# Kernel tuning notes

Hardware: AMD Instinct MI355X
Metric: run time of the kernel (lower is better)

Reference implementation:

```python
import jax, jax.numpy as jnp
import numpy as np
from jax import lax

NUM_EXPERT = 2   # top-k experts kept per image
N_EXPERTS = 4    # total experts


def setup_inputs() -> dict:
    key = jax.random.key(0)
    ks = jax.random.split(key, 4)
    B, C, H, W = 16, 64, 128, 128
    inputs = jax.random.normal(ks[0], (B, C, H, W), dtype=jnp.float32)
    k = jax.random.uniform(ks[1], (B, C, 1, 1), dtype=jnp.float32)
    gate_w = jax.random.normal(ks[2], (N_EXPERTS, C), dtype=jnp.float32) * (1.0 / np.sqrt(C))
    gate_b = jnp.zeros((N_EXPERTS,), dtype=jnp.float32)
    conv_w = jax.random.normal(ks[3], (N_EXPERTS, C, C, 3, 3), dtype=jnp.float32) * (1.0 / np.sqrt(C * 9))
    conv_b = jnp.zeros((N_EXPERTS, C), dtype=jnp.float32)
    return {"inputs": inputs, "k": k, "gate_w": gate_w, "gate_b": gate_b,
            "conv_w": conv_w, "conv_b": conv_b}


def _expert(x, k, w, b):
    # expert_i(x, k) = ReLU(Conv3x3_i(x) + b_i) * k   (FiLM-style conditioning)
    y = lax.conv_general_dilated(x, w, window_strides=(1, 1), padding='SAME',
                                 dimension_numbers=('NCHW', 'OIHW', 'NCHW'))
    return jax.nn.relu(y + b[None, :, None, None]) * k


def reference(inputs, k, gate_w, gate_b, conv_w, conv_b):
    B = inputs.shape[0]
    # gate: global average pool over HW, then linear C -> E
    pooled = inputs.mean(axis=(2, 3))                       # [B, C]
    logits = pooled @ gate_w.T + gate_b                     # [B, E]
    # softmax in float32 (matches F.softmax(..., dtype=torch.float))
    weights = jax.nn.softmax(logits.astype(jnp.float32), axis=1).astype(inputs.dtype)
    topk_w, topk_idx = lax.top_k(weights, NUM_EXPERT)       # [B, num_expert]
    # scatter top-k weights into a dense [B, E] mask (zeros elsewhere)
    exp_weights = jnp.zeros_like(weights).at[jnp.arange(B)[:, None], topk_idx].set(topk_w)
    # dense loop over ALL experts, weighted sum with mostly-zero weights
    out = inputs
    for i in range(N_EXPERTS):
        out = out + _expert(inputs, k, conv_w[i], conv_b[i]) * exp_weights[:, i, None, None, None]
    return out
```

## Files before the change

### kernel.cpp

```cpp
#include <hip/hip_runtime.h>

typedef __attribute__((ext_vector_type(8))) short bfrag8;
typedef __attribute__((ext_vector_type(4))) short bfrag4;
typedef __attribute__((ext_vector_type(16))) float f32x16;

#define B_ 16
#define C_ 64
#define H_ 128
#define W_ 128
#define E_ 4
#define HW_ (H_ * W_)

#define NSL 66
#define PLANE2 (NSL * 16)
#define ROWB2  (8 * PLANE2)
#define RGK 16

#define WT_ELEMS (4 * 9 * 2 * 4 * 64 * 8)
#define OFF_POOL (WT_ELEMS * 2)
#define OFF_EW   (OFF_POOL + 1024 * 4)
#define WS_NEEDED ((size_t)(OFF_EW + 64 * 4))

#define FB_WT_OFF 0
#define FB_POOLED_OFF 147456
#define FB_EW_OFF 148480

__device__ inline unsigned short f2bf(float f) {
    unsigned u = __builtin_bit_cast(unsigned, f);
    unsigned r = u + 0x7FFFu + ((u >> 16) & 1u);
    return (unsigned short)(r >> 16);
}
__device__ inline float bf2f(unsigned short s) {
    return __builtin_bit_cast(float, (unsigned)s << 16);
}

__global__ __launch_bounds__(256) void pool_wcvt(const float* __restrict__ in,
                                                 const float* __restrict__ cw,
                                                 float* __restrict__ pooled,
                                                 unsigned short* __restrict__ wT2) {
    if (blockIdx.x < 576) {
        const int idx = blockIdx.x * 256 + threadIdx.x;
        const int j = idx & 7;
        const int l = (idx >> 3) & 63;
        const int f = idx >> 9;
        const int kb = f & 3;
        const int chh = (f >> 2) & 1;
        const int et = f >> 3;
        const int tap = et % 9;
        const int e = et / 9;
        const int co = chh * 32 + (l & 31);
        const int ci = kb * 16 + (l >> 5) * 8 + j;
        wT2[idx] = f2bf(cw[(((e * C_ + co) * C_ + ci) * 9) + tap]);
    }
    const int bc = blockIdx.x;
    const float* p = in + (size_t)bc * HW_;
    float s = 0.f;
    for (int i = threadIdx.x; i < HW_ / 4; i += 256) {
        float4 v = ((const float4*)p)[i];
        s += v.x + v.y + v.z + v.w;
    }
    for (int off = 32; off; off >>= 1) s += __shfl_down(s, off);
    __shared__ float red[4];
    const int lane = threadIdx.x & 63, wv = threadIdx.x >> 6;
    if (lane == 0) red[wv] = s;
    __syncthreads();
    if (threadIdx.x == 0)
        pooled[bc] = (red[0] + red[1] + red[2] + red[3]) * (1.0f / (float)HW_);
}

__global__ void gate_kernel(const float* __restrict__ pooled,
                            const float* __restrict__ gate_w,
                            const float* __restrict__ gate_b,
                            float* __restrict__ ew) {
    const int b = threadIdx.x;
    if (b >= B_) return;
    float lg[E_];
    for (int e = 0; e < E_; e++) {
        float s = gate_b[e];
        for (int c = 0; c < C_; c++) s += pooled[b * C_ + c] * gate_w[e * C_ + c];
        lg[e] = s;
    }
    float m = fmaxf(fmaxf(lg[0], lg[1]), fmaxf(lg[2], lg[3]));
    float ex[E_], sum = 0.f;
    for (int e = 0; e < E_; e++) { ex[e] = expf(lg[e] - m); sum += ex[e]; }
    for (int e = 0; e < E_; e++) ex[e] /= sum;
    int i1 = 0;
    for (int e = 1; e < E_; e++) if (ex[e] > ex[i1]) i1 = e;
    int i2 = -1;
    for (int e = 0; e < E_; e++) {
        if (e == i1) continue;
        if (i2 < 0 || ex[e] > ex[i2]) i2 = e;
    }
    for (int e = 0; e < E_; e++)
        ew[b * E_ + e] = (e == i1 || e == i2) ? ex[e] : 0.f;
}

__global__ __launch_bounds__(512, 1) void conv_pin(const float* __restrict__ in,
                                                   const float* __restrict__ kk,
                                                   const float* __restrict__ cb,
                                                   const float* __restrict__ pooled,
                                                   const float* __restrict__ gw,
                                                   const float* __restrict__ gb,
                                                   const unsigned short* __restrict__ wT2,
                                                   float* __restrict__ out) {
    const int raw = blockIdx.x;
    const int swz = (raw & 7) * 32 + (raw >> 3);
    const int b   = swz >> 4;
    const int pxh = (swz >> 3) & 1;
    const int h0  = (swz & 7) * RGK;
    const int x0g = pxh * 64;

    const int tid = threadIdx.x;
    const int lane = tid & 63;
    const int wv = tid >> 6;
    const int ln = lane & 31;
    const int lh = lane >> 5;
    const int ei = wv >> 2;
    const int ch = (wv >> 1) & 1;
    const int pq = wv & 1;
    const int co0 = ch * 32;

    const int spx = tid & 63;
    const int scg = tid >> 6;

    __shared__ __align__(16) char ring[3 * ROWB2];
    __shared__ float pbuf[2 * 2 * 32 * 32];
    __shared__ float sEW[E_];

    if (tid < 64) {
        const float p = pooled[b * C_ + lane];
        float part[E_];
#pragma unroll
        for (int e = 0; e < E_; e++) part[e] = p * gw[e * C_ + lane];
#pragma unroll
        for (int off = 32; off; off >>= 1)
#pragma unroll
            for (int e = 0; e < E_; e++) part[e] += __shfl_down(part[e], off);
        if (lane == 0) {
            float lg[E_];
#pragma unroll
            for (int e = 0; e < E_; e++) lg[e] = part[e] + gb[e];
            float m = fmaxf(fmaxf(lg[0], lg[1]), fmaxf(lg[2], lg[3]));
            float ex[E_], sum = 0.f;
#pragma unroll
            for (int e = 0; e < E_; e++) { ex[e] = __expf(lg[e] - m); sum += ex[e]; }
            const float inv = 1.0f / sum;
            int i1 = 0;
            for (int e = 1; e < E_; e++) if (ex[e] > ex[i1]) i1 = e;
            int i2 = -1;
            for (int e = 0; e < E_; e++) {
                if (e == i1) continue;
                if (i2 < 0 || ex[e] > ex[i2]) i2 = e;
            }
#pragma unroll
            for (int e = 0; e < E_; e++)
                sEW[e] = (e == i1 || e == i2) ? ex[e] * inv : 0.f;
        }
    }
    __syncthreads();

    int e0 = 0, e1 = 0; float w0 = 0.f, w1 = 0.f;
    {
        int found = 0;
        for (int e = 0; e < E_; e++) {
            float we = sEW[e];
            if (we != 0.f) {
                if (!found) { e0 = e; w0 = we; found = 1; }
                else        { e1 = e; w1 = we; }
            }
        }
        if (w1 == 0.f) e1 = e0;
    }

    const int es = ei ? e1 : e0;
    const float ww = ei ? w1 : w0;
    const float* cbp = cb + es * C_;
    const float* kkp = kk + b * C_;

    bfrag8 wr[9][4];
    {
        const char* wb = (const char*)wT2 + (size_t)es * 73728 + ch * 4096 + lane * 16;
#pragma unroll
        for (int tap = 0; tap < 9; ++tap)
#pragma unroll
            for (int kb = 0; kb < 4; ++kb)
                wr[tap][kb] = *(const bfrag8*)(wb + tap * 8192 + kb * 1024);
    }
#pragma unroll
    for (int tap = 0; tap < 9; ++tap)
#pragma unroll
        for (int kb = 0; kb < 4; ++kb)
            asm volatile("" : "+v"(wr[tap][kb]));

    float pv[8], ph[8];
    auto STAGE = [&](int r) {
        if ((unsigned)r < (unsigned)H_) {
            const float* src = in + ((size_t)(b * C_ + scg * 8) * H_ + r) * W_ + x0g + spx;
#pragma unroll
            for (int i = 0; i < 8; ++i) pv[i] = src[(size_t)i * HW_];
        } else {
#pragma unroll
            for (int i = 0; i < 8; ++i) pv[i] = 0.f;
        }
        if (tid < 16) {
            const int hp = tid & 1;
            const int cgh = tid >> 1;
            const int pg = hp ? (x0g + 64) : (x0g - 1);
            const bool ok = ((unsigned)r < (unsigned)H_) && ((unsigned)pg < (unsigned)W_);
            const float* src = in + ((size_t)(b * C_ + cgh * 8) * H_ + (((unsigned)r < (unsigned)H_) ? r : 0)) * W_ + (ok ? pg : 0);
#pragma unroll
            for (int i = 0; i < 8; ++i) ph[i] = ok ? src[(size_t)i * HW_] : 0.f;
        }
    };
    auto COMMIT = [&](int rs) {
        bfrag8 f;
#pragma unroll
        for (int i = 0; i < 8; ++i) f[i] = (short)f2bf(pv[i]);
        *(bfrag8*)(ring + rs * ROWB2 + scg * PLANE2 + (spx + 1) * 16) = f;
        if (tid < 16) {
            const int hp = tid & 1, cgh = tid >> 1;
            bfrag8 g;
#pragma unroll
            for (int i = 0; i < 8; ++i) g[i] = (short)f2bf(ph[i]);
            *(bfrag8*)(ring + rs * ROWB2 + cgh * PLANE2 + (hp ? 65 : 0) * 16) = g;
        }
    };

    STAGE(h0 - 1); COMMIT(0);
    STAGE(h0);     COMMIT(1);
    STAGE(h0 + 1); COMMIT(2);
    __syncthreads();

    float* pb = pbuf + (ch * 2 + pq) * 1024;

    int m0 = 0, m1 = 1, m2 = 2;
    for (int s = 0; s < RGK; ++s) {
        if (s + 1 < RGK) STAGE(h0 + s + 2);

        f32x16 A;
#pragma unroll
        for (int i = 0; i < 16; ++i) A[i] = 0.f;

#pragma unroll
        for (int ky = 0; ky < 3; ++ky) {
            const char* rb = ring + (ky == 0 ? m0 : (ky == 1 ? m1 : m2)) * ROWB2;
#pragma unroll
            for (int kx = 0; kx < 3; ++kx) {
#pragma unroll
                for (int kb = 0; kb < 4; ++kb) {
                    bfrag8 bb = *(const bfrag8*)(rb + (kb * 2 + lh) * PLANE2
                                                 + (pq * 32 + ln + kx) * 16);
                    A = __builtin_amdgcn_mfma_f32_32x32x16_bf16(wr[ky * 3 + kx][kb], bb, A, 0, 0, 0);
                }
            }
        }

        __syncthreads();
        if (s + 1 < RGK) COMMIT(m0);

        const int row = h0 + s;
        if (ei == 1) {
#pragma unroll
            for (int g = 0; g < 16; ++g) {
                const int cs = (g & 3) + 8 * (g >> 2) + 4 * lh;
                const int co = co0 + cs;
                const float kv = kkp[co];
                pb[cs * 32 + ln] = fmaxf(A[g] + cbp[co], 0.f) * (kv * ww);
            }
        }
        __syncthreads();
        if (ei == 0) {
            const char* rm1 = ring + m1 * ROWB2 + (pq * 32 + ln + 1) * 16 + lh * 8;
            bfrag4 ra[4];
#pragma unroll
            for (int c = 0; c < 4; ++c)
                ra[c] = *(const bfrag4*)(rm1 + (ch * 4 + c) * PLANE2);
#pragma unroll
            for (int g = 0; g < 16; ++g) {
                const int r_ = g & 3, c_ = g >> 2;
                const int cs = r_ + 8 * c_ + 4 * lh;
                const int co = co0 + cs;
                const float kv = kkp[co];
                const size_t oi = ((size_t)(b * C_ + co) * H_ + row) * W_ + x0g + pq * 32 + ln;
                out[oi] = bf2f((unsigned short)ra[c_][r_])
                          + fmaxf(A[g] + cbp[co], 0.f) * (kv * ww)
                          + pb[cs * 32 + ln];
            }
        }
        const int t = m0; m0 = m1; m1 = m2; m2 = t;
    }
}

#define CHUNK 32

__global__ __launch_bounds__(256) void pool_kernel(const float* __restrict__ in,
                                                   float* __restrict__ pooled) {
    const int bc = blockIdx.x;
    const float* p = in + (size_t)bc * HW_;
    float s = 0.f;
    for (int i = threadIdx.x; i < HW_ / 4; i += 256) {
        float4 v = ((const float4*)p)[i];
        s += v.x + v.y + v.z + v.w;
    }
    for (int off = 32; off; off >>= 1) s += __shfl_down(s, off);
    __shared__ float red[4];
    const int lane = threadIdx.x & 63, wv = threadIdx.x >> 6;
    if (lane == 0) red[wv] = s;
    __syncthreads();
    if (threadIdx.x == 0)
        pooled[bc] = (red[0] + red[1] + red[2] + red[3]) * (1.0f / (float)HW_);
}

__global__ __launch_bounds__(256) void wtr_kernel(const float* __restrict__ cw,
                                                  float* __restrict__ wT) {
    const int idx = blockIdx.x * 256 + threadIdx.x;
    if (idx >= E_ * C_ * 9 * C_) return;
    const int co = idx & 63;
    const int t2 = idx >> 6;
    const int tap = t2 % 9;
    const int t3 = t2 / 9;
    const int ci = t3 & 63;
    const int e = t3 >> 6;
    wT[idx] = cw[(((e * C_ + co) * C_ + ci) * 9) + tap];
}

__global__ __launch_bounds__(512) void conv_fallback(const float* __restrict__ in,
                                                     const float* __restrict__ kk,
                                                     const float* __restrict__ wT,
                                                     const float* __restrict__ cb,
                                                     const float* __restrict__ ew,
                                                     float* __restrict__ out) {
    const int bid = blockIdx.x;
    const int b = bid / H_;
    const int h = bid % H_;
    const int tid = threadIdx.x;
    const int lane = tid & 63;
    const int wv = tid >> 6;
    const int x0 = wv * 16;

    __shared__ float sIn[CHUNK * 3 * W_];

    float w0 = 0.f, w1 = 0.f;
    int e0 = 0, e1 = 0;
    {
        float we[E_];
#pragma unroll
        for (int e = 0; e < E_; e++) we[e] = ew[b * E_ + e];
        int found = 0;
        for (int e = 0; e < E_; e++) {
            if (we[e] != 0.f) {
                if (!found) { e0 = e; w0 = we[e]; found = 1; }
                else        { e1 = e; w1 = we[e]; }
            }
        }
        if (w1 == 0.f) e1 = e0;
    }

    float acc0[16], acc1[16];
#pragma unroll
    for (int i = 0; i < 16; i++) { acc0[i] = 0.f; acc1[i] = 0.f; }

    for (int cblk = 0; cblk < C_ / CHUNK; cblk++) {
        const int cbase = cblk * CHUNK;
        __syncthreads();
        for (int f = tid; f < CHUNK * 3 * W_ / 4; f += 512) {
            const int fi = f * 4;
            const int ci = fi / (3 * W_);
            const int rem = fi - ci * 3 * W_;
            const int kyy = rem / W_;
            const int x = rem - kyy * W_;
            const int hh = h + kyy - 1;
            float4 v = make_float4(0.f, 0.f, 0.f, 0.f);
            if (hh >= 0 && hh < H_)
                v = *(const float4*)(in + ((size_t)(b * C_ + cbase + ci) * H_ + hh) * W_ + x);
            *(float4*)(sIn + fi) = v;
        }
        __syncthreads();

        const float* wp0 = wT + (size_t)((e0 * C_ + cbase) * 9) * C_ + lane;
        const float* wp1 = wT + (size_t)((e1 * C_ + cbase) * 9) * C_ + lane;
        for (int ci = 0; ci < CHUNK; ci++) {
            float wa[9], wb[9];
#pragma unroll
            for (int t = 0; t < 9; t++) {
                wa[t] = wp0[(ci * 9 + t) * C_];
                wb[t] = wp1[(ci * 9 + t) * C_];
            }
            const float* rowp = sIn + ci * 3 * W_;
#pragma unroll
            for (int kyy = 0; kyy < 3; kyy++) {
                float xin[18];
                const float* rp = rowp + kyy * W_ + x0;
                xin[0] = (x0 == 0) ? 0.f : rp[-1];
#pragma unroll
                for (int j = 0; j < 16; j += 4) {
                    float4 v = *(const float4*)(rp + j);
                    xin[1 + j] = v.x; xin[2 + j] = v.y; xin[3 + j] = v.z; xin[4 + j] = v.w;
                }
                xin[17] = (x0 + 16 >= W_) ? 0.f : rp[16];
                const int t0 = kyy * 3;
#pragma unroll
                for (int x = 0; x < 16; x++) {
                    acc0[x] += xin[x] * wa[t0] + xin[x + 1] * wa[t0 + 1] + xin[x + 2] * wa[t0 + 2];
                    acc1[x] += xin[x] * wb[t0] + xin[x + 1] * wb[t0 + 1] + xin[x + 2] * wb[t0 + 2];
                }
            }
        }
    }

    const float kv = kk[b * C_ + lane];
    const float b0v = cb[e0 * C_ + lane];
    const float b1v = cb[e1 * C_ + lane];
    const float kw0 = kv * w0, kw1 = kv * w1;
    const size_t obase = ((size_t)(b * C_ + lane) * H_ + h) * W_ + x0;
#pragma unroll
    for (int x = 0; x < 16; x += 4) {
        float4 iv = *(const float4*)(in + obase + x);
        float4 ov;
        ov.x = iv.x + fmaxf(acc0[x + 0] + b0v, 0.f) * kw0 + fmaxf(acc1[x + 0] + b1v, 0.f) * kw1;
        ov.y = iv.y + fmaxf(acc0[x + 1] + b0v, 0.f) * kw0 + fmaxf(acc1[x + 1] + b1v, 0.f) * kw1;
        ov.z = iv.z + fmaxf(acc0[x + 2] + b0v, 0.f) * kw0 + fmaxf(acc1[x + 2] + b1v, 0.f) * kw1;
        ov.w = iv.w + fmaxf(acc0[x + 3] + b0v, 0.f) * kw0 + fmaxf(acc1[x + 3] + b1v, 0.f) * kw1;
        *(float4*)(out + obase + x) = ov;
    }
}

extern "C" void kernel_launch(void* const* d_in, const int* in_sizes, int n_in,
                              void* d_out, int out_size, void* d_ws, size_t ws_size,
                              hipStream_t stream) {
    const float* inputs = (const float*)d_in[0];
    const float* k      = (const float*)d_in[1];
    const float* gate_w = (const float*)d_in[2];
    const float* gate_b = (const float*)d_in[3];
    const float* conv_w = (const float*)d_in[4];
    const float* conv_b = (const float*)d_in[5];
    float* out = (float*)d_out;
    char* wsb = (char*)d_ws;

    if (ws_size >= WS_NEEDED) {
        unsigned short* wT2 = (unsigned short*)wsb;
        float* pooled = (float*)(wsb + OFF_POOL);

        pool_wcvt<<<B_ * C_, 256, 0, stream>>>(inputs, conv_w, pooled, wT2);
        conv_pin<<<256, 512, 0, stream>>>(inputs, k, conv_b, pooled,
                                          gate_w, gate_b, wT2, out);
    } else {
        float* ws = (float*)d_ws;
        float* wTf    = ws + FB_WT_OFF;
        float* pooled = ws + FB_POOLED_OFF;
        float* ewbuf  = ws + FB_EW_OFF;

        pool_kernel<<<B_ * C_, 256, 0, stream>>>(inputs, pooled);
        gate_kernel<<<1, 64, 0, stream>>>(pooled, gate_w, gate_b, ewbuf);
        wtr_kernel<<<(E_ * C_ * 9 * C_ + 255) / 256, 256, 0, stream>>>(conv_w, wTf);
        conv_fallback<<<B_ * H_, 512, 0, stream>>>(inputs, k, wTf, conv_b, ewbuf, out);
    }
}
```

Before: 101.6 us.

## Compute both experts per wave, shrink row groups, drop register-pinned weights

Restructures the conv kernel so each wave computes both selected experts with two accumulators, replacing the old split where half the waves handled each expert and exchanged results through shared memory. Weight fragments are now read from global/L2 inside the MFMA loop rather than pinned in registers, and blocks shrink to 256 threads over 4-row groups (1024 blocks, 2 per CU) with a 4-slot ring that needs only one barrier per row. This targets the shared-memory reduction, the extra barriers and the low occupancy. The cost is repeated weight loads from cache on every tap and more halo row re-staging across the smaller row groups.

```diff
diff --git a/kernel.cpp b/kernel.cpp
--- a/kernel.cpp
+++ b/kernel.cpp
@@ -14,7 +14,7 @@
 #define NSL 66
 #define PLANE2 (NSL * 16)
 #define ROWB2  (8 * PLANE2)
-#define RGK 16
+#define RG 4
 
 #define WT_ELEMS (4 * 9 * 2 * 4 * 64 * 8)
 #define OFF_POOL (WT_ELEMS * 2)
@@ -95,19 +95,19 @@
         ew[b * E_ + e] = (e == i1 || e == i2) ? ex[e] : 0.f;
 }
 
-__global__ __launch_bounds__(512, 1) void conv_pin(const float* __restrict__ in,
-                                                   const float* __restrict__ kk,
-                                                   const float* __restrict__ cb,
-                                                   const float* __restrict__ pooled,
-                                                   const float* __restrict__ gw,
-                                                   const float* __restrict__ gb,
-                                                   const unsigned short* __restrict__ wT2,
-                                                   float* __restrict__ out) {
+__global__ __launch_bounds__(256, 2) void conv_p4(const float* __restrict__ in,
+                                                  const float* __restrict__ kk,
+                                                  const float* __restrict__ cb,
+                                                  const float* __restrict__ pooled,
+                                                  const float* __restrict__ gw,
+                                                  const float* __restrict__ gb,
+                                                  const unsigned short* __restrict__ wT2,
+                                                  float* __restrict__ out) {
     const int raw = blockIdx.x;
-    const int swz = (raw & 7) * 32 + (raw >> 3);
-    const int b   = swz >> 4;
-    const int pxh = (swz >> 3) & 1;
-    const int h0  = (swz & 7) * RGK;
+    const int swz = (raw & 7) * 128 + (raw >> 3);
+    const int b   = swz >> 6;
+    const int pxh = (swz >> 5) & 1;
+    const int h0  = (swz & 31) * RG;
     const int x0g = pxh * 64;
 
     const int tid = threadIdx.x;
@@ -115,16 +115,14 @@
     const int wv = tid >> 6;
     const int ln = lane & 31;
     const int lh = lane >> 5;
-    const int ei = wv >> 2;
-    const int ch = (wv >> 1) & 1;
-    const int pq = wv & 1;
+    const int ch = wv & 1;
+    const int pq = wv >> 1;
     const int co0 = ch * 32;
 
     const int spx = tid & 63;
     const int scg = tid >> 6;
 
-    __shared__ __align__(16) char ring[3 * ROWB2];
-    __shared__ float pbuf[2 * 2 * 32 * 32];
+    __shared__ __align__(16) char ring[4 * ROWB2];
     __shared__ float sEW[E_];
 
     if (tid < 64) {
@@ -172,35 +170,19 @@
         if (w1 == 0.f) e1 = e0;
     }
 
-    const int es = ei ? e1 : e0;
-    const float ww = ei ? w1 : w0;
-    const float* cbp = cb + es * C_;
+    const float* cb0 = cb + e0 * C_;
+    const float* cb1 = cb + e1 * C_;
     const float* kkp = kk + b * C_;
 
-    bfrag8 wr[9][4];
-    {
-        const char* wb = (const char*)wT2 + (size_t)es * 73728 + ch * 4096 + lane * 16;
-#pragma unroll
-        for (int tap = 0; tap < 9; ++tap)
-#pragma unroll
-            for (int kb = 0; kb < 4; ++kb)
-                wr[tap][kb] = *(const bfrag8*)(wb + tap * 8192 + kb * 1024);
-    }
-#pragma unroll
-    for (int tap = 0; tap < 9; ++tap)
-#pragma unroll
-        for (int kb = 0; kb < 4; ++kb)
-            asm volatile("" : "+v"(wr[tap][kb]));
-
-    float pv[8], ph[8];
+    float pv[16], ph[8];
     auto STAGE = [&](int r) {
         if ((unsigned)r < (unsigned)H_) {
-            const float* src = in + ((size_t)(b * C_ + scg * 8) * H_ + r) * W_ + x0g + spx;
-#pragma unroll
-            for (int i = 0; i < 8; ++i) pv[i] = src[(size_t)i * HW_];
+            const float* src = in + ((size_t)(b * C_ + scg * 16) * H_ + r) * W_ + x0g + spx;
+#pragma unroll
+            for (int i = 0; i < 16; ++i) pv[i] = src[(size_t)i * HW_];
         } else {
 #pragma unroll
-            for (int i = 0; i < 8; ++i) pv[i] = 0.f;
+            for (int i = 0; i < 16; ++i) pv[i] = 0.f;
         }
         if (tid < 16) {
             const int hp = tid & 1;
@@ -213,10 +195,15 @@
         }
     };
     auto COMMIT = [&](int rs) {
-        bfrag8 f;
-#pragma unroll
-        for (int i = 0; i < 8; ++i) f[i] = (short)f2bf(pv[i]);
-        *(bfrag8*)(ring + rs * ROWB2 + scg * PLANE2 + (spx + 1) * 16) = f;
+        bfrag8 f0, f1;
+#pragma unroll
+        for (int j = 0; j < 8; ++j) {
+            f0[j] = (short)f2bf(pv[j]);
+            f1[j] = (short)f2bf(pv[8 + j]);
+        }
+        char* bp = ring + rs * ROWB2 + (spx + 1) * 16;
+        *(bfrag8*)(bp + (scg * 2) * PLANE2) = f0;
+        *(bfrag8*)(bp + (scg * 2 + 1) * PLANE2) = f1;
         if (tid < 16) {
             const int hp = tid & 1, cgh = tid >> 1;
             bfrag8 g;
@@ -231,63 +218,54 @@
     STAGE(h0 + 1); COMMIT(2);
     __syncthreads();
 
-    float* pb = pbuf + (ch * 2 + pq) * 1024;
-
-    int m0 = 0, m1 = 1, m2 = 2;
-    for (int s = 0; s < RGK; ++s) {
-        if (s + 1 < RGK) STAGE(h0 + s + 2);
-
-        f32x16 A;
-#pragma unroll
-        for (int i = 0; i < 16; ++i) A[i] = 0.f;
+    const char* wb0 = (const char*)wT2 + (size_t)e0 * 73728 + ch * 4096 + lane * 16;
+    const char* wb1 = (const char*)wT2 + (size_t)e1 * 73728 + ch * 4096 + lane * 16;
+
+    for (int s = 0; s < RG; ++s) {
+        if (s + 1 < RG) STAGE(h0 + s + 2);
+
+        f32x16 Ae0, Ae1;
+#pragma unroll
+        for (int i = 0; i < 16; ++i) { Ae0[i] = 0.f; Ae1[i] = 0.f; }
 
 #pragma unroll
         for (int ky = 0; ky < 3; ++ky) {
-            const char* rb = ring + (ky == 0 ? m0 : (ky == 1 ? m1 : m2)) * ROWB2;
+            const char* rb = ring + ((s + ky) & 3) * ROWB2;
 #pragma unroll
             for (int kx = 0; kx < 3; ++kx) {
+                const int tap = ky * 3 + kx;
 #pragma unroll
                 for (int kb = 0; kb < 4; ++kb) {
+                    bfrag8 a0 = *(const bfrag8*)(wb0 + tap * 8192 + kb * 1024);
+                    bfrag8 a1 = *(const bfrag8*)(wb1 + tap * 8192 + kb * 1024);
                     bfrag8 bb = *(const bfrag8*)(rb + (kb * 2 + lh) * PLANE2
                                                  + (pq * 32 + ln + kx) * 16);
-                    A = __builtin_amdgcn_mfma_f32_32x32x16_bf16(wr[ky * 3 + kx][kb], bb, A, 0, 0, 0);
+                    Ae0 = __builtin_amdgcn_mfma_f32_32x32x16_bf16(a0, bb, Ae0, 0, 0, 0);
+                    Ae1 = __builtin_amdgcn_mfma_f32_32x32x16_bf16(a1, bb, Ae1, 0, 0, 0);
                 }
             }
         }
 
+        if (s + 1 < RG) COMMIT((s + 3) & 3);
+
+        const int row = h0 + s;
+        const char* rm1 = ring + ((s + 1) & 3) * ROWB2 + (pq * 32 + ln + 1) * 16 + lh * 8;
+        bfrag4 ra[4];
+#pragma unroll
+        for (int c = 0; c < 4; ++c)
+            ra[c] = *(const bfrag4*)(rm1 + (ch * 4 + c) * PLANE2);
+#pragma unroll
+        for (int g = 0; g < 16; ++g) {
+            const int r_ = g & 3, c_ = g >> 2;
+            const int co = co0 + r_ + 8 * c_ + 4 * lh;
+            const float kv = kkp[co];
+            const size_t oi = ((size_t)(b * C_ + co) * H_ + row) * W_ + x0g + pq * 32 + ln;
+            out[oi] = bf2f((unsigned short)ra[c_][r_])
+                      + fmaxf(Ae0[g] + cb0[co], 0.f) * (kv * w0)
+                      + fmaxf(Ae1[g] + cb1[co], 0.f) * (kv * w1);
+        }
+
         __syncthreads();
-        if (s + 1 < RGK) COMMIT(m0);
-
-        const int row = h0 + s;
-        if (ei == 1) {
-#pragma unroll
-            for (int g = 0; g < 16; ++g) {
-                const int cs = (g & 3) + 8 * (g >> 2) + 4 * lh;
-                const int co = co0 + cs;
-                const float kv = kkp[co];
-                pb[cs * 32 + ln] = fmaxf(A[g] + cbp[co], 0.f) * (kv * ww);
-            }
-        }
-        __syncthreads();
-        if (ei == 0) {
-            const char* rm1 = ring + m1 * ROWB2 + (pq * 32 + ln + 1) * 16 + lh * 8;
-            bfrag4 ra[4];
-#pragma unroll
-            for (int c = 0; c < 4; ++c)
-                ra[c] = *(const bfrag4*)(rm1 + (ch * 4 + c) * PLANE2);
-#pragma unroll
-            for (int g = 0; g < 16; ++g) {
-                const int r_ = g & 3, c_ = g >> 2;
-                const int cs = r_ + 8 * c_ + 4 * lh;
-                const int co = co0 + cs;
-                const float kv = kkp[co];
-                const size_t oi = ((size_t)(b * C_ + co) * H_ + row) * W_ + x0g + pq * 32 + ln;
-                out[oi] = bf2f((unsigned short)ra[c_][r_])
-                          + fmaxf(A[g] + cbp[co], 0.f) * (kv * ww)
-                          + pb[cs * 32 + ln];
-            }
-        }
-        const int t = m0; m0 = m1; m1 = m2; m2 = t;
     }
 }
 
@@ -442,7 +420,7 @@
         float* pooled = (float*)(wsb + OFF_POOL);
 
         pool_wcvt<<<B_ * C_, 256, 0, stream>>>(inputs, conv_w, pooled, wT2);
-        conv_pin<<<256, 512, 0, stream>>>(inputs, k, conv_b, pooled,
+        conv_p4<<<1024, 256, 0, stream>>>(inputs, k, conv_b, pooled,
                                           gate_w, gate_b, wT2, out);
     } else {
         float* ws = (float*)d_ws;
```

After: 337.0 us. 232% more time.
